# Kernel tuning notes

Hardware: AMD Instinct MI355X
Metric: run time of the kernel (lower is better)

The kernel has to match this reference:

```python
import jax, jax.numpy as jnp
from jax import lax
import numpy as np

EMA_ALPHA = 0.3
LN_EPS = 1e-5
SW = 5  # center_window_size


def _gelu(x):
    return jax.nn.gelu(x, approximate=False)  # torch nn.GELU default = exact erf


def _layernorm(x, g, b):
    mu = x.mean(-1, keepdims=True)
    var = ((x - mu) ** 2).mean(-1, keepdims=True)
    return (x - mu) * lax.rsqrt(var + LN_EPS) * g + b


def _ema_scan(x, alpha):
    # x: [B, T, C]; x_smooth[t] = lerp(x_smooth[t-1], x[t], alpha)
    x0 = x[:, 0]
    def step(prev, xt):
        s = prev + alpha * (xt - prev)
        return s, s
    _, ys = lax.scan(step, x0, jnp.swapaxes(x[:, 1:], 0, 1))  # [T-1, B, C]
    return jnp.concatenate([x0[:, None], jnp.swapaxes(ys, 0, 1)], axis=1)


def _lstm_dir(x, w_ih, w_hh, b):
    # x: [B, T, Cin]; w_ih: [Cin, 4H]; w_hh: [H, 4H]; b: [4H]. torch gate order i,f,g,o
    B = x.shape[0]
    H = w_hh.shape[0]
    pre = jnp.einsum('btc,ch->bth', x, w_ih) + b  # [B, T, 4H]
    def step(carry, p):
        h, c = carry
        gates = p + h @ w_hh
        i, f, g, o = jnp.split(gates, 4, axis=-1)
        c = jax.nn.sigmoid(f) * c + jax.nn.sigmoid(i) * jnp.tanh(g)
        h = jax.nn.sigmoid(o) * jnp.tanh(c)
        return (h, c), h
    init = (jnp.zeros((B, H), x.dtype), jnp.zeros((B, H), x.dtype))
    _, hs = lax.scan(step, init, jnp.swapaxes(pre, 0, 1))  # [T, B, H]
    return jnp.swapaxes(hs, 0, 1)


def _bilstm(x, wih_f, whh_f, b_f, wih_r, whh_r, b_r):
    fwd = _lstm_dir(x, wih_f, whh_f, b_f)
    bwd = jnp.flip(_lstm_dir(jnp.flip(x, axis=1), wih_r, whh_r, b_r), axis=1)
    return jnp.concatenate([fwd, bwd], axis=-1)  # [B, T, 2H]


def setup_inputs() -> dict:
    key = jax.random.key(0)
    ks = jax.random.split(key, 24)
    B, T, C, BD, O, H = 4096, 31, 768, 128, 12, 64
    AUG = 3 * BD  # 384
    def n(k, shape, s):
        return jax.random.normal(k, shape, dtype=jnp.float32) * s
    return {
        'x': n(ks[0], (B, T, C), 1.0),
        'cls_w': n(ks[1], (C, BD), 0.03), 'cls_b': jnp.zeros((BD,), jnp.float32),
        'delta_w': n(ks[2], (C, BD), 0.03), 'delta_b': jnp.zeros((BD,), jnp.float32),
        'acc_w': n(ks[3], (C, BD), 0.03), 'acc_b': jnp.zeros((BD,), jnp.float32),
        'cls_ln_g': jnp.ones((BD,), jnp.float32), 'cls_ln_b': jnp.zeros((BD,), jnp.float32),
        'delta_ln_g': jnp.ones((BD,), jnp.float32), 'delta_ln_b': jnp.zeros((BD,), jnp.float32),
        'acc_ln_g': jnp.ones((BD,), jnp.float32), 'acc_ln_b': jnp.zeros((BD,), jnp.float32),
        'lin0_w': n(ks[4], (AUG, 256), 0.05), 'lin0_b': jnp.zeros((256,), jnp.float32),
        'gate': jnp.float32(0.2),
        'attn_w': n(ks[5], (2 * H, 1), 0.08), 'attn_b': jnp.zeros((1,), jnp.float32),
        'attn_temp': jnp.float32(1.0),
        'lin1_w': n(ks[6], (C, O), 0.03), 'lin1_b': jnp.zeros((O,), jnp.float32),
        'lin2_w': n(ks[7], (2 * H, O), 0.08), 'lin2_b': jnp.zeros((O,), jnp.float32),
        'lstm_wih_f': n(ks[8], (256, 4 * H), 0.06), 'lstm_whh_f': n(ks[9], (H, 4 * H), 0.12),
        'lstm_b_f': jnp.zeros((4 * H,), jnp.float32),
        'lstm_wih_r': n(ks[10], (256, 4 * H), 0.06), 'lstm_whh_r': n(ks[11], (H, 4 * H), 0.12),
        'lstm_b_r': jnp.zeros((4 * H,), jnp.float32),
    }


def reference(x, cls_w, cls_b, delta_w, delta_b, acc_w, acc_b,
              cls_ln_g, cls_ln_b, delta_ln_g, delta_ln_b, acc_ln_g, acc_ln_b,
              lin0_w, lin0_b, gate, attn_w, attn_b, attn_temp,
              lin1_w, lin1_b, lin2_w, lin2_b,
              lstm_wih_f, lstm_whh_f, lstm_b_f, lstm_wih_r, lstm_whh_r, lstm_b_r):
    T = x.shape[1]
    hsl = T // 2
    l, r = max(0, hsl - SW), min(T, hsl + SW + 1)  # center window [10, 21) for T=31

    # --- robust deltas: EMA smoothing + reflect-padded finite differences ---
    x_smooth = _ema_scan(x, EMA_ALPHA)                       # [B, T, C]
    padded = jnp.pad(x_smooth, ((0, 0), (2, 0), (0, 0)), mode='reflect')  # [B, T+2, C]
    dx = padded[:, 1:] - padded[:, :-1]                       # [B, T+1, C]
    ddx = dx[:, 1:] - dx[:, :-1]                              # [B, T, C]
    delta_stream = dx[:, 1:]                                  # [B, T, C]
    acc_stream = ddx                                          # [B, T, C]

    # --- linear branch: mean of lin1 over center window of smoothed stream ---
    linear_logits = (x_smooth[:, l:r] @ lin1_w + lin1_b).mean(axis=1)  # [B, O]

    # --- bottlenecks (eval mode: dropout identity) + LayerNorms ---
    cls_bn = _layernorm(_gelu(x_smooth @ cls_w + cls_b), cls_ln_g, cls_ln_b)
    delta_bn = _layernorm(_gelu(delta_stream @ delta_w + delta_b), delta_ln_g, delta_ln_b)
    acc_bn = _layernorm(_gelu(acc_stream @ acc_w + acc_b), acc_ln_g, acc_ln_b)
    x_aug = jnp.concatenate([cls_bn, delta_bn, acc_bn], axis=-1)  # [B, T, 384]

    x_lstm = _gelu(x_aug @ lin0_w + lin0_b)                   # [B, T, 256]
    x_lstm = x_lstm - x_lstm.mean(axis=1, keepdims=True)      # center over time (fp32)

    # --- BiLSTM + attention pooling over center window ---
    lstm_out = _bilstm(x_lstm, lstm_wih_f, lstm_whh_f, lstm_b_f,
                       lstm_wih_r, lstm_whh_r, lstm_b_r)      # [B, T, 128]
    window = lstm_out[:, l:r]                                 # [B, W, 128]
    temp = jax.nn.softplus(attn_temp) + 0.001
    scores = (window @ attn_w + attn_b)[..., 0] / temp        # [B, W]
    attn = jax.nn.softmax(scores, axis=1)[..., None]          # [B, W, 1]
    attended = (attn * window).sum(axis=1)                    # [B, 128]
    lstm_logits = attended @ lin2_w + lin2_b                  # [B, O]

    g = jax.nn.sigmoid(gate)
    final_logits = linear_logits + g * (lstm_logits - linear_logits)
    return final_logits, attended
```

## Files before the change

kernel.cpp:

```cpp
#include <hip/hip_runtime.h>
#include <cstdint>
#include <cstddef>


typedef short s8v __attribute__((ext_vector_type(8)));
typedef float f4v __attribute__((ext_vector_type(4)));

#if defined(__has_builtin)
#if __has_builtin(__builtin_amdgcn_global_load_lds)
#define HAVE_GLL 1
#endif
#endif
#ifndef HAVE_GLL
#define HAVE_GLL 0
#endif

__device__ __forceinline__ unsigned short f2bf(float f) {
  union { float f; unsigned int u; } v; v.f = f;
  unsigned int u = v.u;
  return (unsigned short)((u + 0x7fffu + ((u >> 16) & 1u)) >> 16);
}
__device__ __forceinline__ float bf2f(unsigned short h) {
  union { unsigned int u; float f; } v; v.u = ((unsigned int)h) << 16;
  return v.f;
}
__device__ __forceinline__ float fsig(float x) {
  return __fdividef(1.f, 1.f + __expf(-x));
}
__device__ __forceinline__ float ftanh(float x) {
  return 1.f - __fdividef(2.f, 1.f + __expf(2.f * x));
}
__device__ __forceinline__ float fgelu(float x) {
  return 0.5f * x * (1.f + erff(x * 0.70710678118654752f));
}

__device__ __forceinline__ void ld_lds16(const unsigned short* g,
                                         unsigned short* ldsU, int lane) {
#if HAVE_GLL
  __builtin_amdgcn_global_load_lds(
      (__attribute__((address_space(1))) void*)(uintptr_t)(const void*)g,
      (__attribute__((address_space(3))) void*)(unsigned int)(uintptr_t)(void*)ldsU,
      16, 0, 0);
#else
  *(uint4*)(ldsU + lane * 8) = *(const uint4*)g;
#endif
}
__device__ __forceinline__ void wait_vm0() {
#if HAVE_GLL
  __builtin_amdgcn_s_waitcnt(0x0F70);
#endif
}

#define OFF_W1T   0u
#define OFF_W2T   589824u
#define OFF_WIHT  786432u
#define OFF_WHHT  1048576u
#define OFF_XS    1114112u
#define OFF_XW    196149248u
#define OFF_LL    208732160u
#define OFF_WIN   208928768u
#define OFF_XAUG  220463104u
#define OFF_XLSTM 317980672u

__global__ __launch_bounds__(256) void k0_prep(
    const float* __restrict__ cls_w, const float* __restrict__ delta_w,
    const float* __restrict__ acc_w, const float* __restrict__ lin0_w,
    const float* __restrict__ wih_f, const float* __restrict__ wih_r,
    const float* __restrict__ whh_f, const float* __restrict__ whh_r,
    unsigned short* __restrict__ ws) {
  int i = blockIdx.x * 256 + threadIdx.x;
  if (i < 294912) {
    int n = i / 768, k = i - n * 768;
    int seg = n >> 7, nn = n & 127;
    const float* w = seg == 0 ? cls_w : (seg == 1 ? delta_w : acc_w);
    ws[i] = f2bf(w[k * 128 + nn]);
  } else if (i < 393216) {
    int j = i - 294912;
    int n = j / 384, k = j - n * 384;
    ws[i] = f2bf(lin0_w[k * 256 + n]);
  } else if (i < 524288) {
    int j = i - 393216;
    int n = j >> 8, k = j & 255;
    ws[i] = f2bf(n < 256 ? wih_f[k * 256 + n] : wih_r[k * 256 + (n - 256)]);
  } else if (i < 557056) {
    int j = i - 524288;
    int d = j >> 14, rem = j & 16383;
    int n = rem >> 6, k = rem & 63;
    const float* w = d ? whh_r : whh_f;
    ws[i] = f2bf(w[k * 256 + n]);
  }
}

__global__ __launch_bounds__(256) void k1_ema(
    const float* __restrict__ x, unsigned short* __restrict__ xs,
    float* __restrict__ xw) {
  int gid = blockIdx.x * 256 + threadIdx.x;
  int b = gid / 768;
  int c = gid - b * 768;
  size_t base = (size_t)b * 31 * 768 + c;
  float s = x[base];
  xs[base] = f2bf(s);
  float wsum = 0.f;
#pragma unroll
  for (int t = 1; t < 31; ++t) {
    float xv = x[base + t * 768];
    s = s + 0.3f * (xv - s);
    xs[base + t * 768] = f2bf(s);
    if (t >= 10 && t <= 20) wsum += s;
  }
  xw[gid] = wsum * (1.f / 11.f);
}

__global__ __launch_bounds__(64) void k1b_linlog(
    const float* __restrict__ xw, const float* __restrict__ lin1_w,
    const float* __restrict__ lin1_b, float* __restrict__ ll) {
  int b = blockIdx.x;
  int lane = threadIdx.x;
  float p[12];
#pragma unroll
  for (int o = 0; o < 12; ++o) p[o] = 0.f;
  for (int k = lane; k < 768; k += 64) {
    float xv = xw[b * 768 + k];
    const float* w = lin1_w + k * 12;
#pragma unroll
    for (int o = 0; o < 12; ++o) p[o] += xv * w[o];
  }
#pragma unroll
  for (int o = 0; o < 12; ++o) {
    float v = p[o];
#pragma unroll
    for (int s = 1; s < 64; s <<= 1) v += __shfl_xor(v, s, 64);
    p[o] = v;
  }
  if (lane == 0) {
#pragma unroll
    for (int o = 0; o < 12; ++o) ll[b * 12 + o] = p[o] + lin1_b[o];
  }
}

template <int KDIM>
__device__ __forceinline__ void gemm128(
    const unsigned short* __restrict__ A, int rowClamp,
    const unsigned short* __restrict__ Bt,
    unsigned short* sA, unsigned short* sB, f4v acc[4][4]) {
  const int tid  = threadIdx.x;
  const int lane = tid & 63;
  const int wv   = tid >> 6;
  const int l15  = lane & 15;
  const int quad = lane >> 4;
  const int mh   = (wv >> 1) * 64;
  const int nh   = (wv & 1) * 64;

  const int srow = wv * 32 + (lane >> 3);
  const int scol = (lane & 7) * 8;
  const unsigned short* aBase[4];
  const unsigned short* bBase[4];
  unsigned short* aDst[4];
  unsigned short* bDst[4];
#pragma unroll
  for (int j = 0; j < 4; ++j) {
    int r = srow + j * 8;
    int ar = r < rowClamp ? r : rowClamp;
    aBase[j] = A + (size_t)ar * KDIM + scol;
    bBase[j] = Bt + (size_t)r * KDIM + scol;
    aDst[j] = sA + (wv * 4 + j) * 512;
    bDst[j] = sB + (wv * 4 + j) * 512;
  }
#pragma unroll
  for (int mt = 0; mt < 4; ++mt)
#pragma unroll
    for (int nt = 0; nt < 4; ++nt)
      acc[mt][nt] = (f4v){0.f, 0.f, 0.f, 0.f};

  constexpr int KT = KDIM / 64;
  for (int kt = 0; kt < KT; ++kt) {
    if (kt) __syncthreads();
    int ko = kt * 64;
#pragma unroll
    for (int j = 0; j < 4; ++j) ld_lds16(aBase[j] + ko, aDst[j], lane);
#pragma unroll
    for (int j = 0; j < 4; ++j) ld_lds16(bBase[j] + ko, bDst[j], lane);
    wait_vm0();
    __syncthreads();
#pragma unroll
    for (int ks = 0; ks < 2; ++ks) {
      s8v af[4], bfv[4];
#pragma unroll
      for (int mt = 0; mt < 4; ++mt)
        af[mt] = *(const s8v*)(&sA[(mh + mt * 16 + l15) * 64 + ks * 32 + quad * 8]);
#pragma unroll
      for (int nt = 0; nt < 4; ++nt)
        bfv[nt] = *(const s8v*)(&sB[(nh + nt * 16 + l15) * 64 + ks * 32 + quad * 8]);
#pragma unroll
      for (int mt = 0; mt < 4; ++mt)
#pragma unroll
        for (int nt = 0; nt < 4; ++nt)
          acc[mt][nt] = __builtin_amdgcn_mfma_f32_16x16x32_bf16(af[mt], bfv[nt], acc[mt][nt], 0, 0, 0);
    }
  }
  __syncthreads();
}

__device__ __forceinline__ void dump_chunk(f4v acc[4][4], float* sP, int lo,
                                           int nrows, int pstr) {
  const int tid  = threadIdx.x;
  const int lane = tid & 63;
  const int wv   = tid >> 6;
  const int l15  = lane & 15;
  const int quad = lane >> 4;
  const int mh   = (wv >> 1) * 64;
  const int nh   = (wv & 1) * 64;
#pragma unroll
  for (int mt = 0; mt < 4; ++mt)
#pragma unroll
    for (int nt = 0; nt < 4; ++nt)
#pragma unroll
      for (int r = 0; r < 4; ++r) {
        int rr = mh + mt * 16 + quad * 4 + r - lo;
        if ((unsigned)rr < (unsigned)nrows)
          sP[rr * pstr + nh + nt * 16 + l15] = acc[mt][nt][r];
      }
}

__device__ __forceinline__ float stencil_gelu(const float* sP, int seg, int row, int t,
                                              int col, const float* __restrict__ bias) {
  const float* p = sP + row * 132 + col;
  float v;
  if (seg == 0) {
    v = p[0];
  } else if (seg == 1) {
    v = (t == 0) ? (p[0] - p[132]) : (p[0] - p[-132]);
  } else {
    if (t == 0)      v = p[0] - 2.f * p[132] + p[264];
    else if (t == 1) v = 2.f * (p[0] - p[-132]);
    else             v = p[0] - 2.f * p[-132] + p[-264];
  }
  return fgelu(v + bias[col]);
}

__global__ __launch_bounds__(256) void k2_aug(
    const unsigned short* __restrict__ xs, const unsigned short* __restrict__ W1t,
    const float* __restrict__ cls_b, const float* __restrict__ delta_b,
    const float* __restrict__ acc_b,
    const float* __restrict__ g0, const float* __restrict__ be0,
    const float* __restrict__ g1, const float* __restrict__ be1,
    const float* __restrict__ g2, const float* __restrict__ be2,
    unsigned short* __restrict__ xaug) {
  __shared__ __align__(16) char smem[33280];
  unsigned short* sA = (unsigned short*)smem;
  unsigned short* sB = (unsigned short*)(smem + 16384);
  float* sP  = (float*)smem;
  float* sMu = (float*)(smem + 32768);
  float* sRs = sMu + 62;
  int seg = blockIdx.y;
  int rowBase = blockIdx.x * 124;
  f4v acc[4][4];
  gemm128<768>(xs + (size_t)rowBase * 768, 123, W1t + (size_t)seg * 128 * 768, sA, sB, acc);
  const float* bias = seg == 0 ? cls_b : (seg == 1 ? delta_b : acc_b);
  const float* lng  = seg == 0 ? g0 : (seg == 1 ? g1 : g2);
  const float* lnb  = seg == 0 ? be0 : (seg == 1 ? be1 : be2);
  int tid = threadIdx.x;
#pragma unroll
  for (int ck = 0; ck < 2; ++ck) {
    int lo = ck * 62;
    dump_chunk(acc, sP, lo, 62, 132);
    __syncthreads();
    if (tid < 248) {
      int row = tid >> 2, q = tid & 3;
      int t = row % 31;
      float sum = 0.f, ss = 0.f;
      for (int i = 0; i < 32; ++i) {
        float v = stencil_gelu(sP, seg, row, t, q + 4 * i, bias);
        sum += v; ss += v * v;
      }
      sum += __shfl_xor(sum, 1, 64); sum += __shfl_xor(sum, 2, 64);
      ss  += __shfl_xor(ss,  1, 64); ss  += __shfl_xor(ss,  2, 64);
      float mu = sum * (1.f / 128.f);
      if (q == 0) { sMu[row] = mu; sRs[row] = rsqrtf(ss * (1.f / 128.f) - mu * mu + 1e-5f); }
    }
    __syncthreads();
    for (int idx = tid; idx < 62 * 128; idx += 256) {
      int row = idx >> 7, col = idx & 127;
      int t = row % 31;
      float v = stencil_gelu(sP, seg, row, t, col, bias);
      float o = (v - sMu[row]) * sRs[row] * lng[col] + lnb[col];
      xaug[(size_t)(rowBase + lo + row) * 384 + seg * 128 + col] = f2bf(o);
    }
    __syncthreads();
  }
}

__global__ __launch_bounds__(256) void k3_lstm_in(
    const unsigned short* __restrict__ xaug, const unsigned short* __restrict__ W2t,
    const float* __restrict__ lin0_b, unsigned short* __restrict__ xlstm) {
  __shared__ __align__(16) char smem[33792];
  unsigned short* sA = (unsigned short*)smem;
  unsigned short* sB = (unsigned short*)(smem + 16384);
  float* sP  = (float*)smem;
  float* sCM = (float*)(smem + 32768);
  int by = blockIdx.y;
  int rowBase = blockIdx.x * 124;
  f4v acc[4][4];
  gemm128<384>(xaug + (size_t)rowBase * 384, 123, W2t + (size_t)by * 128 * 384, sA, sB, acc);
  int tid = threadIdx.x;
#pragma unroll
  for (int ck = 0; ck < 2; ++ck) {
    int lo = ck * 62;
    dump_chunk(acc, sP, lo, 62, 132);
    __syncthreads();
    for (int idx = tid; idx < 62 * 128; idx += 256) {
      int row = idx >> 7, col = idx & 127;
      sP[row * 132 + col] = fgelu(sP[row * 132 + col] + lin0_b[by * 128 + col]);
    }
    __syncthreads();
    {
      int bb = tid >> 7, col = tid & 127;
      float s = 0.f;
      for (int tr = 0; tr < 31; ++tr) s += sP[(bb * 31 + tr) * 132 + col];
      sCM[tid] = s * (1.f / 31.f);
    }
    __syncthreads();
    for (int idx = tid; idx < 62 * 128; idx += 256) {
      int row = idx >> 7, col = idx & 127;
      int bb = row >= 31 ? 1 : 0;
      float v = sP[row * 132 + col] - sCM[bb * 128 + col];
      xlstm[(size_t)(rowBase + lo + row) * 256 + by * 128 + col] = f2bf(v);
    }
    __syncthreads();
  }
}

__global__ __launch_bounds__(256) void k3b_pre(
    const unsigned short* __restrict__ xlstm, const unsigned short* __restrict__ Wiht,
    const float* __restrict__ b_f, const float* __restrict__ b_r,
    unsigned short* __restrict__ pre) {
  __shared__ __align__(16) char smem[32768];
  unsigned short* sA = (unsigned short*)smem;
  unsigned short* sB = (unsigned short*)(smem + 16384);
  float* sP = (float*)smem;
  int by = blockIdx.y;
  int rowBase = blockIdx.x * 128;
  f4v acc[4][4];
  gemm128<256>(xlstm + (size_t)rowBase * 256, 127, Wiht + (size_t)by * 128 * 256, sA, sB, acc);
  int tid = threadIdx.x;
#pragma unroll
  for (int ck = 0; ck < 2; ++ck) {
    int lo = ck * 64;
    dump_chunk(acc, sP, lo, 64, 128);
    __syncthreads();
    for (int idx = tid; idx < 64 * 128; idx += 256) {
      int row = idx >> 7, col = idx & 127;
      int gcol = by * 128 + col;
      float bias = gcol < 256 ? b_f[gcol] : b_r[gcol - 256];
      pre[(size_t)(rowBase + lo + row) * 512 + gcol] = f2bf(sP[row * 128 + col] + bias);
    }
    __syncthreads();
  }
}

__global__ __launch_bounds__(256) void k4_lstm(
    const unsigned short* __restrict__ pre, const unsigned short* __restrict__ Whht,
    unsigned short* __restrict__ win) {
  __shared__ unsigned short sW[256 * 72];
  __shared__ unsigned short sH[16 * 72];
  __shared__ float sG[16 * 260];
  int tid = threadIdx.x;
  int dir = blockIdx.y;
  int b0  = blockIdx.x * 16;
  {
    const unsigned short* src = Whht + dir * 16384;
#pragma unroll
    for (int c = 0; c < 8; ++c) {
      int id = tid + c * 256;
      int row = id >> 3, kc = (id & 7) * 8;
      uint4 v = *(const uint4*)(src + row * 64 + kc);
      *(uint4*)(&sW[row * 72 + kc]) = v;
    }
  }
  for (int i = tid; i < 16 * 72; i += 256) sH[i] = 0;
  __syncthreads();

  const int lane = tid & 63, wv = tid >> 6, l15 = lane & 15, quad = lane >> 4;
  const int eb = tid >> 4, jb = (tid & 15) * 4;
  float cs[4] = {0.f, 0.f, 0.f, 0.f};

  int tt0 = dir ? 30 : 0;
  const unsigned short* pbase = pre + ((size_t)(b0 + eb) * 31) * 512 + dir * 256;
  ushort4 pi = *(const ushort4*)(pbase + tt0 * 512 + jb);
  ushort4 pf = *(const ushort4*)(pbase + tt0 * 512 + 64 + jb);
  ushort4 pg = *(const ushort4*)(pbase + tt0 * 512 + 128 + jb);
  ushort4 po = *(const ushort4*)(pbase + tt0 * 512 + 192 + jb);

  for (int t = 0; t < 31; ++t) {
    f4v acc[4];
#pragma unroll
    for (int nt = 0; nt < 4; ++nt) acc[nt] = (f4v){0.f, 0.f, 0.f, 0.f};
#pragma unroll
    for (int ks = 0; ks < 2; ++ks) {
      s8v af = *(const s8v*)(&sH[l15 * 72 + ks * 32 + quad * 8]);
#pragma unroll
      for (int nt = 0; nt < 4; ++nt) {
        int n = wv * 64 + nt * 16 + l15;
        s8v bfv = *(const s8v*)(&sW[n * 72 + ks * 32 + quad * 8]);
        acc[nt] = __builtin_amdgcn_mfma_f32_16x16x32_bf16(af, bfv, acc[nt], 0, 0, 0);
      }
    }
#pragma unroll
    for (int nt = 0; nt < 4; ++nt)
#pragma unroll
      for (int r = 0; r < 4; ++r)
        sG[(quad * 4 + r) * 260 + wv * 64 + nt * 16 + l15] = acc[nt][r];

    ushort4 ni, nf, ng, no;
    if (t < 30) {
      int ttn = dir ? 29 - t : t + 1;
      ni = *(const ushort4*)(pbase + ttn * 512 + jb);
      nf = *(const ushort4*)(pbase + ttn * 512 + 64 + jb);
      ng = *(const ushort4*)(pbase + ttn * 512 + 128 + jb);
      no = *(const ushort4*)(pbase + ttn * 512 + 192 + jb);
    }
    __syncthreads();

    int tt = dir ? 30 - t : t;
    const float* g = &sG[eb * 260];
    float hv[4];
#pragma unroll
    for (int jj = 0; jj < 4; ++jj) {
      int j = jb + jj;
      float vi = g[j]       + bf2f(jj == 0 ? pi.x : jj == 1 ? pi.y : jj == 2 ? pi.z : pi.w);
      float vf = g[64 + j]  + bf2f(jj == 0 ? pf.x : jj == 1 ? pf.y : jj == 2 ? pf.z : pf.w);
      float vg = g[128 + j] + bf2f(jj == 0 ? pg.x : jj == 1 ? pg.y : jj == 2 ? pg.z : pg.w);
      float vo = g[192 + j] + bf2f(jj == 0 ? po.x : jj == 1 ? po.y : jj == 2 ? po.z : po.w);
      float cc = fsig(vf) * cs[jj] + fsig(vi) * ftanh(vg);
      cs[jj] = cc;
      hv[jj] = fsig(vo) * ftanh(cc);
    }
    ushort4 hb;
    hb.x = f2bf(hv[0]); hb.y = f2bf(hv[1]); hb.z = f2bf(hv[2]); hb.w = f2bf(hv[3]);
    *(ushort4*)(&sH[eb * 72 + jb]) = hb;
    if (tt >= 10 && tt <= 20)
      *(ushort4*)(win + ((size_t)(b0 + eb) * 11 + (tt - 10)) * 128 + dir * 64 + jb) = hb;
    if (t < 30) { pi = ni; pf = nf; pg = ng; po = no; }
    __syncthreads();
  }
}

__global__ __launch_bounds__(256) void k5_attn(
    const unsigned short* __restrict__ win, const float* __restrict__ attn_w,
    const float* __restrict__ attn_b, const float* __restrict__ attn_t,
    const float* __restrict__ lin2_w, const float* __restrict__ lin2_b,
    const float* __restrict__ linlog, const float* __restrict__ gate,
    float* __restrict__ out) {
  __shared__ unsigned short sWin[176 * 128];
  __shared__ float sAw[128];
  __shared__ float sSc[176];
  __shared__ float sAtt[16 * 128];
  int tid = threadIdx.x;
  int b0  = blockIdx.x * 16;
#pragma unroll
  for (int c = 0; c < 11; ++c) {
    int id = tid + c * 256;
    int row = id >> 4, kc = (id & 15) * 8;
    uint4 v = *(const uint4*)(win + ((size_t)b0 * 11 + row) * 128 + kc);
    *(uint4*)(&sWin[row * 128 + kc]) = v;
  }
  if (tid < 128) sAw[tid] = attn_w[tid];
  __syncthreads();
  if (tid < 176) {
    int b = tid / 11, wt = tid - b * 11;
    const unsigned short* w = &sWin[(b * 11 + wt) * 128];
    float dot = 0.f;
    for (int ch = 0; ch < 128; ++ch) dot += bf2f(w[ch]) * sAw[ch];
    float temp = logf(1.f + __expf(attn_t[0])) + 0.001f;
    sSc[tid] = (dot + attn_b[0]) / temp;
  }
  __syncthreads();
  if (tid < 16) {
    float m = -1e30f;
    for (int wt = 0; wt < 11; ++wt) m = fmaxf(m, sSc[tid * 11 + wt]);
    float e[11], sum = 0.f;
    for (int wt = 0; wt < 11; ++wt) { e[wt] = __expf(sSc[tid * 11 + wt] - m); sum += e[wt]; }
    float inv = __fdividef(1.f, sum);
    for (int wt = 0; wt < 11; ++wt) sSc[tid * 11 + wt] = e[wt] * inv;
  }
  __syncthreads();
#pragma unroll
  for (int p = 0; p < 8; ++p) {
    int task = tid + p * 256;
    int b = task >> 7, ch = task & 127;
    float a = 0.f;
    for (int wt = 0; wt < 11; ++wt)
      a += sSc[b * 11 + wt] * bf2f(sWin[(b * 11 + wt) * 128 + ch]);
    sAtt[b * 128 + ch] = a;
    out[49152 + (size_t)(b0 + b) * 128 + ch] = a;
  }
  __syncthreads();
  if (tid < 192) {
    int b = tid / 12, o = tid - b * 12;
    float dot = 0.f;
    for (int ch = 0; ch < 128; ++ch) dot += sAtt[b * 128 + ch] * lin2_w[ch * 12 + o];
    dot += lin2_b[o];
    float lin = linlog[(size_t)(b0 + b) * 12 + o];
    float gg = fsig(gate[0]);
    out[(size_t)(b0 + b) * 12 + o] = lin + gg * (dot - lin);
  }
}

extern "C" void kernel_launch(void* const* d_in, const int* in_sizes, int n_in,
                              void* d_out, int out_size, void* d_ws, size_t ws_size,
                              hipStream_t stream) {
  const float* x       = (const float*)d_in[0];
  const float* cls_w   = (const float*)d_in[1];
  const float* cls_b   = (const float*)d_in[2];
  const float* delta_w = (const float*)d_in[3];
  const float* delta_b = (const float*)d_in[4];
  const float* acc_w   = (const float*)d_in[5];
  const float* acc_b   = (const float*)d_in[6];
  const float* cls_g   = (const float*)d_in[7];
  const float* cls_be  = (const float*)d_in[8];
  const float* del_g   = (const float*)d_in[9];
  const float* del_be  = (const float*)d_in[10];
  const float* accg    = (const float*)d_in[11];
  const float* accbe   = (const float*)d_in[12];
  const float* lin0_w  = (const float*)d_in[13];
  const float* lin0_b  = (const float*)d_in[14];
  const float* gate    = (const float*)d_in[15];
  const float* attn_w  = (const float*)d_in[16];
  const float* attn_b  = (const float*)d_in[17];
  const float* attn_t  = (const float*)d_in[18];
  const float* lin1_w  = (const float*)d_in[19];
  const float* lin1_b  = (const float*)d_in[20];
  const float* lin2_w  = (const float*)d_in[21];
  const float* lin2_b  = (const float*)d_in[22];
  const float* wih_f   = (const float*)d_in[23];
  const float* whh_f   = (const float*)d_in[24];
  const float* b_f     = (const float*)d_in[25];
  const float* wih_r   = (const float*)d_in[26];
  const float* whh_r   = (const float*)d_in[27];
  const float* b_r     = (const float*)d_in[28];

  char* ws = (char*)d_ws;
  unsigned short* W1t   = (unsigned short*)(ws + OFF_W1T);
  unsigned short* W2t   = (unsigned short*)(ws + OFF_W2T);
  unsigned short* Wiht  = (unsigned short*)(ws + OFF_WIHT);
  unsigned short* Whht  = (unsigned short*)(ws + OFF_WHHT);
  unsigned short* XS    = (unsigned short*)(ws + OFF_XS);
  unsigned short* PRE   = XS;
  float*          XW    = (float*)(ws + OFF_XW);
  float*          LL    = (float*)(ws + OFF_LL);
  unsigned short* WIN   = (unsigned short*)(ws + OFF_WIN);
  unsigned short* XAUG  = (unsigned short*)(ws + OFF_XAUG);
  unsigned short* XLSTM = (unsigned short*)(ws + OFF_XLSTM);
  float* out = (float*)d_out;

  k0_prep<<<2176, 256, 0, stream>>>(cls_w, delta_w, acc_w, lin0_w, wih_f, wih_r,
                                    whh_f, whh_r, (unsigned short*)ws);
  k1_ema<<<12288, 256, 0, stream>>>(x, XS, XW);
  k1b_linlog<<<4096, 64, 0, stream>>>(XW, lin1_w, lin1_b, LL);
  k2_aug<<<dim3(1024, 3), 256, 0, stream>>>(XS, W1t, cls_b, delta_b, acc_b,
                                            cls_g, cls_be, del_g, del_be, accg, accbe, XAUG);
  k3_lstm_in<<<dim3(1024, 2), 256, 0, stream>>>(XAUG, W2t, lin0_b, XLSTM);
  k3b_pre<<<dim3(992, 4), 256, 0, stream>>>(XLSTM, Wiht, b_f, b_r, PRE);
  k4_lstm<<<dim3(256, 2), 256, 0, stream>>>(PRE, Whht, WIN);
  k5_attn<<<256, 256, 0, stream>>>(WIN, attn_w, attn_b, attn_t, lin2_w, lin2_b,
                                   LL, gate, out);
}
```

Before: 1.131 ms.

## Merge k2_aug segments into one 1024-thread block computing 124x384 tile

Rewrites k2_aug so a single 1024-thread block computes all three 128-column segments (N=384) for its 124 rows, instead of three separate blocks each reloading the same 124x768 A tile. The GEMM is now inline with double-buffered LDS (64 KB per stage), a swizzled layout, and 16 waves arranged 2x8. The epilogue processes 31-row chunks for all segments at once, with bias and LN params cached in LDS. This removes the triple read of XS from global memory, at the cost of 128 KB of LDS per block and lower occupancy (one block per CU).

New measurement: 1.101 ms. -2.7%, faster.

```diff
diff --git a/kernel.cpp b/kernel.cpp
--- a/kernel.cpp
+++ b/kernel.cpp
@@ -222,23 +222,23 @@
       }
 }
 
-__device__ __forceinline__ float stencil_gelu(const float* sP, int seg, int row, int t,
-                                              int col, const float* __restrict__ bias) {
-  const float* p = sP + row * 132 + col;
+__device__ __forceinline__ float stencil_gelu3(const float* sP, const float* sBias,
+                                               int seg, int t, int c) {
+  const float* p = sP + t * 390 + seg * 130 + c;
   float v;
   if (seg == 0) {
     v = p[0];
   } else if (seg == 1) {
-    v = (t == 0) ? (p[0] - p[132]) : (p[0] - p[-132]);
+    v = (t == 0) ? (p[0] - p[390]) : (p[0] - p[-390]);
   } else {
-    if (t == 0)      v = p[0] - 2.f * p[132] + p[264];
-    else if (t == 1) v = 2.f * (p[0] - p[-132]);
-    else             v = p[0] - 2.f * p[-132] + p[-264];
-  }
-  return fgelu(v + bias[col]);
-}
-
-__global__ __launch_bounds__(256) void k2_aug(
+    if (t == 0)      v = p[0] - 2.f * p[390] + p[780];
+    else if (t == 1) v = 2.f * (p[0] - p[-390]);
+    else             v = p[0] - 2.f * p[-390] + p[-780];
+  }
+  return fgelu(v + sBias[seg * 128 + c]);
+}
+
+__global__ __launch_bounds__(1024) void k2_aug(
     const unsigned short* __restrict__ xs, const unsigned short* __restrict__ W1t,
     const float* __restrict__ cls_b, const float* __restrict__ delta_b,
     const float* __restrict__ acc_b,
@@ -246,45 +246,132 @@
     const float* __restrict__ g1, const float* __restrict__ be1,
     const float* __restrict__ g2, const float* __restrict__ be2,
     unsigned short* __restrict__ xaug) {
-  __shared__ __align__(16) char smem[33280];
-  unsigned short* sA = (unsigned short*)smem;
-  unsigned short* sB = (unsigned short*)(smem + 16384);
-  float* sP  = (float*)smem;
-  float* sMu = (float*)(smem + 32768);
-  float* sRs = sMu + 62;
-  int seg = blockIdx.y;
-  int rowBase = blockIdx.x * 124;
-  f4v acc[4][4];
-  gemm128<768>(xs + (size_t)rowBase * 768, 123, W1t + (size_t)seg * 128 * 768, sA, sB, acc);
-  const float* bias = seg == 0 ? cls_b : (seg == 1 ? delta_b : acc_b);
-  const float* lng  = seg == 0 ? g0 : (seg == 1 ? g1 : g2);
-  const float* lnb  = seg == 0 ? be0 : (seg == 1 ? be1 : be2);
-  int tid = threadIdx.x;
-#pragma unroll
-  for (int ck = 0; ck < 2; ++ck) {
-    int lo = ck * 62;
-    dump_chunk(acc, sP, lo, 62, 132);
-    __syncthreads();
-    if (tid < 248) {
-      int row = tid >> 2, q = tid & 3;
-      int t = row % 31;
+  __shared__ __align__(16) char smem[131072];
+  unsigned short* buf0 = (unsigned short*)smem;
+  unsigned short* buf1 = (unsigned short*)(smem + 65536);
+  float* sP    = (float*)smem;
+  float* sBias = (float*)(smem + 65536);
+  float* sG    = sBias + 384;
+  float* sLb   = sG + 384;
+  float* sMu   = sLb + 384;
+  float* sRs   = sMu + 93;
+
+  const int tid  = threadIdx.x;
+  const int lane = tid & 63;
+  const int wv   = tid >> 6;
+  const int l15  = lane & 15;
+  const int quad = lane >> 4;
+  const int wm   = wv >> 3;
+  const int wn   = wv & 7;
+  const int rowBase = blockIdx.x * 124;
+
+  const int subrow = lane >> 3;
+  const int schunk = ((lane & 7) ^ subrow) * 8;
+  const unsigned short* src[4];
+#pragma unroll
+  for (int j = 0; j < 4; ++j) {
+    int slice = wv * 4 + j;
+    int row = slice * 8 + subrow;
+    src[j] = (row < 128)
+        ? xs + (size_t)(rowBase + (row < 124 ? row : 123)) * 768 + schunk
+        : W1t + (size_t)(row - 128) * 768 + schunk;
+  }
+
+  f4v acc[4][3];
+#pragma unroll
+  for (int mt = 0; mt < 4; ++mt)
+#pragma unroll
+    for (int nt = 0; nt < 3; ++nt) acc[mt][nt] = (f4v){0.f, 0.f, 0.f, 0.f};
+
+  const int swz = (l15 & 7) << 3;
+
+#pragma unroll
+  for (int j = 0; j < 4; ++j) ld_lds16(src[j], buf0 + (wv * 4 + j) * 512, lane);
+  wait_vm0();
+  __syncthreads();
+
+  for (int kt = 0; kt < 12; ++kt) {
+    unsigned short* bc = (kt & 1) ? buf1 : buf0;
+    unsigned short* bn = (kt & 1) ? buf0 : buf1;
+    if (kt < 11) {
+#pragma unroll
+      for (int j = 0; j < 4; ++j)
+        ld_lds16(src[j] + (kt + 1) * 64, bn + (wv * 4 + j) * 512, lane);
+    }
+#pragma unroll
+    for (int ks = 0; ks < 2; ++ks) {
+      s8v af[4], bfv[3];
+      const int ko = (ks * 32 + quad * 8) ^ swz;
+#pragma unroll
+      for (int mt = 0; mt < 4; ++mt)
+        af[mt] = *(const s8v*)(&bc[(wm * 64 + mt * 16 + l15) * 64 + ko]);
+#pragma unroll
+      for (int nt = 0; nt < 3; ++nt)
+        bfv[nt] = *(const s8v*)(&bc[(128 + wn * 48 + nt * 16 + l15) * 64 + ko]);
+#pragma unroll
+      for (int mt = 0; mt < 4; ++mt)
+#pragma unroll
+        for (int nt = 0; nt < 3; ++nt)
+          acc[mt][nt] = __builtin_amdgcn_mfma_f32_16x16x32_bf16(af[mt], bfv[nt], acc[mt][nt], 0, 0, 0);
+    }
+    wait_vm0();
+    __syncthreads();
+  }
+
+  if (tid < 384) {
+    int seg = tid >> 7, c = tid & 127;
+    sBias[tid] = seg == 0 ? cls_b[c] : (seg == 1 ? delta_b[c] : acc_b[c]);
+    sG[tid]    = seg == 0 ? g0[c]    : (seg == 1 ? g1[c]    : g2[c]);
+    sLb[tid]   = seg == 0 ? be0[c]   : (seg == 1 ? be1[c]   : be2[c]);
+  }
+
+#pragma unroll
+  for (int ck = 0; ck < 4; ++ck) {
+    int lo = ck * 31;
+#pragma unroll
+    for (int mt = 0; mt < 4; ++mt) {
+      int rbase = wm * 64 + mt * 16 + quad * 4 - lo;
+#pragma unroll
+      for (int nt = 0; nt < 3; ++nt) {
+        int gcol = wn * 48 + nt * 16;
+        int colp = (gcol >> 7) * 130 + (gcol & 127) + l15;
+#pragma unroll
+        for (int r = 0; r < 4; ++r) {
+          int rr = rbase + r;
+          if ((unsigned)rr < 31u) sP[rr * 390 + colp] = acc[mt][nt][r];
+        }
+      }
+    }
+    __syncthreads();
+    if (tid < 744) {
+      int seg = tid < 248 ? 0 : (tid < 496 ? 1 : 2);
+      int rem = tid - seg * 248;
+      int row = rem >> 3, q = rem & 7;
       float sum = 0.f, ss = 0.f;
-      for (int i = 0; i < 32; ++i) {
-        float v = stencil_gelu(sP, seg, row, t, q + 4 * i, bias);
+#pragma unroll
+      for (int i = 0; i < 16; ++i) {
+        float v = stencil_gelu3(sP, sBias, seg, row, q + 8 * i);
         sum += v; ss += v * v;
       }
-      sum += __shfl_xor(sum, 1, 64); sum += __shfl_xor(sum, 2, 64);
-      ss  += __shfl_xor(ss,  1, 64); ss  += __shfl_xor(ss,  2, 64);
-      float mu = sum * (1.f / 128.f);
-      if (q == 0) { sMu[row] = mu; sRs[row] = rsqrtf(ss * (1.f / 128.f) - mu * mu + 1e-5f); }
-    }
-    __syncthreads();
-    for (int idx = tid; idx < 62 * 128; idx += 256) {
-      int row = idx >> 7, col = idx & 127;
-      int t = row % 31;
-      float v = stencil_gelu(sP, seg, row, t, col, bias);
-      float o = (v - sMu[row]) * sRs[row] * lng[col] + lnb[col];
-      xaug[(size_t)(rowBase + lo + row) * 384 + seg * 128 + col] = f2bf(o);
+      sum += __shfl_xor(sum, 1, 64); ss += __shfl_xor(ss, 1, 64);
+      sum += __shfl_xor(sum, 2, 64); ss += __shfl_xor(ss, 2, 64);
+      sum += __shfl_xor(sum, 4, 64); ss += __shfl_xor(ss, 4, 64);
+      if (q == 0) {
+        float mu = sum * (1.f / 128.f);
+        sMu[seg * 31 + row] = mu;
+        sRs[seg * 31 + row] = rsqrtf(ss * (1.f / 128.f) - mu * mu + 1e-5f);
+      }
+    }
+    __syncthreads();
+#pragma unroll
+    for (int seg = 0; seg < 3; ++seg) {
+      for (int idx = tid; idx < 31 * 128; idx += 1024) {
+        int row = idx >> 7, c = idx & 127;
+        float v = stencil_gelu3(sP, sBias, seg, row, c);
+        float o = (v - sMu[seg * 31 + row]) * sRs[seg * 31 + row]
+                  * sG[seg * 128 + c] + sLb[seg * 128 + c];
+        xaug[(size_t)(rowBase + lo + row) * 384 + seg * 128 + c] = f2bf(o);
+      }
     }
     __syncthreads();
   }
@@ -557,8 +644,8 @@
                                     whh_f, whh_r, (unsigned short*)ws);
   k1_ema<<<12288, 256, 0, stream>>>(x, XS, XW);
   k1b_linlog<<<4096, 64, 0, stream>>>(XW, lin1_w, lin1_b, LL);
-  k2_aug<<<dim3(1024, 3), 256, 0, stream>>>(XS, W1t, cls_b, delta_b, acc_b,
-                                            cls_g, cls_be, del_g, del_be, accg, accbe, XAUG);
+  k2_aug<<<1024, 1024, 0, stream>>>(XS, W1t, cls_b, delta_b, acc_b,
+                                    cls_g, cls_be, del_g, del_be, accg, accbe, XAUG);
   k3_lstm_in<<<dim3(1024, 2), 256, 0, stream>>>(XAUG, W2t, lin0_b, XLSTM);
   k3b_pre<<<dim3(992, 4), 256, 0, stream>>>(XLSTM, Wiht, b_f, b_r, PRE);
   k4_lstm<<<dim3(256, 2), 256, 0, stream>>>(PRE, Whht, WIN);
```
